# Kernel tuning notes

Hardware: AMD Instinct MI355X
Metric: run time of the kernel (lower is better)

## Reference

```python
import jax, jax.numpy as jnp
import numpy as np

B, N, D = 8, 1024, 256   # batch, nodes, input_size
H, HO = 4, 64            # nhead, hidden_size/nhead
T = 5                    # number of edge types (len(edges))
NEG = -1e9
EPS = 1e-6


def setup_inputs() -> dict:
    key = jax.random.key(0)
    ks = jax.random.split(key, 6)
    nodes_embed = jax.random.normal(ks[0], (B, N, D), dtype=jnp.float32)
    node_adj = jax.random.randint(ks[1], (B, N, N), 0, T + 1)  # values 0..T, 0 = no edge
    # per-head projection W: xavier-ish scale
    W = jax.random.normal(ks[2], (H, D, HO), dtype=jnp.float32) * (1.0 / np.sqrt(D))
    # per-edge-type scoring linear (2*HO -> 1), split into src/dst halves
    a_src = jax.random.normal(ks[3], (H, T, HO), dtype=jnp.float32) * 0.1
    a_dst = jax.random.normal(ks[4], (H, T, HO), dtype=jnp.float32) * 0.1
    bias = jnp.zeros((H, HO), dtype=jnp.float32)
    ln_gamma = jnp.ones((H, HO), dtype=jnp.float32)
    ln_beta = jnp.zeros((H, HO), dtype=jnp.float32)
    return {
        'nodes_embed': nodes_embed,
        'node_adj': node_adj,
        'W': W,
        'a_src': a_src,
        'a_dst': a_dst,
        'bias': bias,
        'ln_gamma': ln_gamma,
        'ln_beta': ln_beta,
    }


def reference(nodes_embed, node_adj, W, a_src, a_dst, bias, ln_gamma, ln_beta):
    # h: [B, H, N, HO] -- all heads projected at once
    h = jnp.einsum('bnd,hde->bhne', nodes_embed, W)
    # The torch code concatenates [h_i, h_j] and applies a (2*HO -> 1) linear per
    # edge type; that equals e_src[t, i] + e_dst[t, j] with the linear weight split
    # into src/dst halves. Avoids materializing the O(N^2 * 2*HO) concat tensor.
    e_src = jnp.einsum('bhne,hte->bhtn', h, a_src)  # [B, H, T, N]
    e_dst = jnp.einsum('bhne,hte->bhtn', h, a_dst)  # [B, H, T, N]
    n_types = a_src.shape[1]
    weight = jnp.zeros(h.shape[:2] + (h.shape[2], h.shape[2]), dtype=h.dtype)  # [B,H,N,N]
    for t in range(n_types):  # small fixed loop over edge types
        mask = (node_adj == t + 1).astype(h.dtype)[:, None]  # [B,1,N,N]
        weight = weight + mask * (e_src[:, :, t, :, None] + e_dst[:, :, t, None, :])
    weight = jax.nn.leaky_relu(weight, negative_slope=0.01)
    weight = jnp.where(node_adj[:, None] == 0, NEG, weight)
    attention = jax.nn.softmax(weight, axis=-1)  # [B,H,N,N]
    dst = jnp.einsum('bhij,bhje->bhie', attention, h) + bias[None, :, None, :]
    out = jax.nn.relu(dst) + h  # dropout is identity (p=0)
    # per-head LayerNorm over HO, eps=1e-6 (biased variance, as torch)
    mu = out.mean(axis=-1, keepdims=True)
    var = out.var(axis=-1, keepdims=True)
    out = (out - mu) / jnp.sqrt(var + EPS) * ln_gamma[None, :, None, :] + ln_beta[None, :, None, :]
    # concat heads: [B,H,N,HO] -> [B,N,H*HO]
    b, hh, n, e = out.shape
    return out.transpose(0, 2, 1, 3).reshape(b, n, hh * e)
```

## Files before the change

kernel.cpp:

```cpp
#include <hip/hip_runtime.h>
#include <hip/hip_bf16.h>

#define Bn 8
#define Nn 1024
#define Dn 256
#define Hn 4
#define HOn 64
#define Tn 5
#define WTR 80
#define EDS 134

typedef short bf16x8 __attribute__((ext_vector_type(8)));
typedef float f32x4 __attribute__((ext_vector_type(4)));

__device__ __forceinline__ float b2f(unsigned short u) {
    unsigned x = ((unsigned)u) << 16;
    float f;
    __builtin_memcpy(&f, &x, 4);
    return f;
}
__device__ __forceinline__ unsigned bfr(float f) {
    unsigned u;
    __builtin_memcpy(&u, &f, 4);
    return (u + 0x7FFFu + ((u >> 16) & 1u)) >> 16;
}
__device__ __forceinline__ unsigned short f2b(float f) { return (unsigned short)bfr(f); }

__device__ __forceinline__ float fast_exp2(float x) {
#if __has_builtin(__builtin_amdgcn_exp2f)
    return __builtin_amdgcn_exp2f(x);
#else
    float r;
    asm("v_exp_f32 %0, %1" : "=v"(r) : "v"(x));
    return r;
#endif
}

__global__ __launch_bounds__(256) void k_signal(float* __restrict__ out, int n) {
    int i = blockIdx.x * 256 + threadIdx.x;
    if (i < n) out[i] = 100.0f;
}

__global__ __launch_bounds__(256) void k_transpose_w(const float* __restrict__ W,
                                                     const float* __restrict__ a_src,
                                                     const float* __restrict__ a_dst,
                                                     unsigned short* __restrict__ WT) {
    __shared__ float tile[64][65];
    int h = blockIdx.x >> 2;
    int d0 = (blockIdx.x & 3) * 64;
    int c0 = threadIdx.x & 63;
    int r0 = threadIdx.x >> 6;
#pragma unroll
    for (int r = 0; r < 16; r++) {
        int d = r * 4 + r0;
        tile[d][c0] = W[((size_t)(h * Dn + d0 + d)) * HOn + c0];
    }
    __syncthreads();
#pragma unroll
    for (int r = 0; r < 16; r++) {
        int e = r * 4 + r0;
        WT[((size_t)(h * WTR + e)) * Dn + d0 + c0] = f2b(tile[c0][e]);
    }
    for (int t = r0; t < 2 * Tn; t += 4) {
        const float* av = (t < Tn) ? (a_src + (h * Tn + t) * HOn)
                                   : (a_dst + (h * Tn + t - Tn) * HOn);
        float s = 0.f;
#pragma unroll
        for (int e = 0; e < HOn; e++) s += tile[c0][e] * av[e];
        WT[((size_t)(h * WTR + 64 + t)) * Dn + d0 + c0] = f2b(s);
    }
    for (int rr = 74 + r0; rr < WTR; rr += 4)
        WT[((size_t)(h * WTR + rr)) * Dn + d0 + c0] = 0;
}

__global__ __launch_bounds__(256) void k_proj(const float* __restrict__ X,
                                              const unsigned short* __restrict__ WT,
                                              const int* __restrict__ adj,
                                              unsigned short* __restrict__ hT,
                                              float* __restrict__ e_src,
                                              float* __restrict__ e_dst,
                                              unsigned* __restrict__ adjp) {
    int tid = threadIdx.x;
    int w = tid >> 6;
    int lane = tid & 63;
    int quad = lane >> 4;
    int l15 = lane & 15;
    int b = blockIdx.x >> 6;
    int i0 = (blockIdx.x & 63) * 16;
    int h = w;
    int bh = b * Hn + h;

    {
        const int* arow = adj + ((size_t)(b * Nn + i0)) * Nn;
        unsigned* aout = adjp + ((size_t)(b * Nn + i0)) * Nn / 4;
#pragma unroll 4
        for (int k = 0; k < 16; k++) {
            int idx = tid + k * 256;
            int4 v = *(const int4*)(arow + (size_t)idx * 4);
            unsigned pk = (unsigned)(v.x & 0xFF) | ((unsigned)(v.y & 0xFF) << 8) |
                          ((unsigned)(v.z & 0xFF) << 16) | ((unsigned)(v.w & 0xFF) << 24);
            aout[idx] = pk;
        }
    }

    bf16x8 Bx[8];
    const float* xf = X + ((size_t)(b * Nn + i0 + l15)) * Dn + quad * 8;
#pragma unroll
    for (int kc = 0; kc < 8; kc++) {
        union { bf16x8 v; unsigned u[4]; } uu;
        const float4* xp = (const float4*)(xf + kc * 32);
        float4 A0 = xp[0], A1 = xp[1];
        __hip_bfloat162 h0 = __float22bfloat162_rn(make_float2(A0.x, A0.y));
        __hip_bfloat162 h1 = __float22bfloat162_rn(make_float2(A0.z, A0.w));
        __hip_bfloat162 h2 = __float22bfloat162_rn(make_float2(A1.x, A1.y));
        __hip_bfloat162 h3 = __float22bfloat162_rn(make_float2(A1.z, A1.w));
        __builtin_memcpy(&uu.u[0], &h0, 4);
        __builtin_memcpy(&uu.u[1], &h1, 4);
        __builtin_memcpy(&uu.u[2], &h2, 4);
        __builtin_memcpy(&uu.u[3], &h3, 4);
        Bx[kc] = uu.v;
    }

    f32x4 acc[5] = {{0.f, 0.f, 0.f, 0.f}, {0.f, 0.f, 0.f, 0.f}, {0.f, 0.f, 0.f, 0.f},
                    {0.f, 0.f, 0.f, 0.f}, {0.f, 0.f, 0.f, 0.f}};
    const unsigned short* wbase = WT + (size_t)h * WTR * Dn;
#pragma unroll
    for (int kc = 0; kc < 8; kc++) {
#pragma unroll
        for (int et = 0; et < 5; et++) {
            bf16x8 Aw = *(const bf16x8*)(wbase + (size_t)(et * 16 + l15) * Dn + kc * 32 + quad * 8);
            acc[et] = __builtin_amdgcn_mfma_f32_16x16x32_bf16(Aw, Bx[kc], acc[et], 0, 0, 0);
        }
    }

#pragma unroll
    for (int et = 0; et < 4; et++) {
#pragma unroll
        for (int reg = 0; reg < 4; reg++) {
            int e = et * 16 + quad * 4 + reg;
            hT[((size_t)bh * HOn + e) * Nn + i0 + l15] = f2b(acc[et][reg]);
        }
    }
#pragma unroll
    for (int reg = 0; reg < 4; reg++) {
        int t = quad * 4 + reg;
        if (t < Tn)
            e_src[((size_t)bh * Tn + t) * Nn + i0 + l15] = acc[4][reg] * 1.4426950408889634f;
        else if (t < 2 * Tn)
            e_dst[((size_t)bh * Tn + (t - Tn)) * Nn + i0 + l15] = acc[4][reg] * 1.4426950408889634f;
    }
}

__global__ __launch_bounds__(512) void k_attn(const unsigned char* __restrict__ adjp,
                                              const float* __restrict__ e_src,
                                              const float* __restrict__ e_dst,
                                              const unsigned short* __restrict__ hT,
                                              const float* __restrict__ bias,
                                              const float* __restrict__ gamma,
                                              const float* __restrict__ beta,
                                              float* __restrict__ out) {
    __shared__ __align__(16) unsigned short p_lds[8][16][136];
    __shared__ float es2[4][16][8];
    __shared__ float l_lds[8][16];
    __shared__ __align__(16) float ed_lds[8][6 * EDS];
    float* macc = (float*)&p_lds[4][0][0];

    int tid = threadIdx.x;
    int w = tid >> 6;
    int lane = tid & 63;
    int quad = lane >> 4;
    int l15 = lane & 15;
    int hh = w & 3;
    int half = w >> 2;
    int b = blockIdx.x >> 6;
    int i0 = (blockIdx.x & 63) * 16;
    int bh = b * Hn + hh;
    int J0 = half * 512;

    const unsigned char* adj_base = adjp + ((size_t)(b * Nn + i0)) * Nn + J0;
    const float* edst = e_dst + (size_t)bh * Tn * Nn + J0;
    const unsigned short* hTb = hT + (size_t)bh * HOn * Nn;

    int c0 = 2 * lane;
    int c0w = c0 + (c0 >> 5);
    float* edw = &ed_lds[w][0];

    f32x4 acc[4] = {{0.f, 0.f, 0.f, 0.f}, {0.f, 0.f, 0.f, 0.f},
                    {0.f, 0.f, 0.f, 0.f}, {0.f, 0.f, 0.f, 0.f}};
    f32x4 accl = {0.f, 0.f, 0.f, 0.f};
    bf16x8 ONES;
    {
        short o = (short)0x3F80;
        ONES = (bf16x8){o, o, o, o, o, o, o, o};
    }

    edw[c0w] = -3e38f;
    edw[c0w + 1] = -3e38f;

    unsigned bufA[4], bufB[4];
#pragma unroll
    for (int r = 0; r < 4; r++)
        bufA[r] = *(const unsigned short*)(adj_base + (size_t)r * Nn + c0);
    float2 edr[Tn];
#pragma unroll
    for (int t = 0; t < Tn; t++) edr[t] = *(const float2*)(edst + t * Nn + c0);

    if (w < 4) {
        const float* esrc = e_src + (size_t)bh * Tn * Nn;
#pragma unroll
        for (int idx = lane; idx < 96; idx += 64) {
            int t = idx >> 4, row = idx & 15;
            es2[w][row][t] = t ? esrc[(t - 1) * Nn + i0 + row] : 0.f;
        }
    }
    __syncthreads();

#define P1ROW(ROW, AV)                                                          \
    {                                                                           \
        int a0 = (int)((AV) & 0xFFu);                                           \
        int a1 = (int)((AV) >> 8);                                              \
        float e0 = es2[hh][ROW][a0];                                            \
        float e1 = es2[hh][ROW][a1];                                            \
        float d0 = edw[a0 * EDS + c0w];                                         \
        float d1 = edw[a1 * EDS + c0w + 1];                                     \
        float x0 = e0 + d0; x0 = fmaxf(x0, 0.01f * x0);                         \
        float x1 = e1 + d1; x1 = fmaxf(x1, 0.01f * x1);                         \
        float p0 = fast_exp2(x0);                                               \
        float p1 = fast_exp2(x1);                                               \
        __hip_bfloat162 pp = __float22bfloat162_rn(make_float2(p0, p1));        \
        unsigned pu; __builtin_memcpy(&pu, &pp, 4);                             \
        *(unsigned*)(&p_lds[w][ROW][2 * lane]) = pu;                            \
    }

#pragma unroll 1
    for (int c = 0; c < 4; c++) {
        int jc = c * 128;
#pragma unroll
        for (int t = 0; t < Tn; t++) {
            int wi = (t + 1) * EDS + c0w;
            edw[wi] = edr[t].x;
            edw[wi + 1] = edr[t].y;
        }
#pragma unroll
        for (int r = 0; r < 4; r++)
            bufB[r] = *(const unsigned short*)(adj_base + (size_t)(4 + r) * Nn + jc + c0);
#pragma unroll
        for (int r = 0; r < 4; r++) P1ROW(r, bufA[r]);
#pragma unroll
        for (int r = 0; r < 4; r++)
            bufA[r] = *(const unsigned short*)(adj_base + (size_t)(8 + r) * Nn + jc + c0);
        if (c < 3) {
#pragma unroll
            for (int t = 0; t < Tn; t++)
                edr[t] = *(const float2*)(edst + t * Nn + jc + 128 + c0);
        }
#pragma unroll
        for (int r = 0; r < 4; r++) P1ROW(4 + r, bufB[r]);
#pragma unroll
        for (int r = 0; r < 4; r++)
            bufB[r] = *(const unsigned short*)(adj_base + (size_t)(12 + r) * Nn + jc + c0);
#pragma unroll
        for (int r = 0; r < 4; r++) P1ROW(8 + r, bufA[r]);
        if (c < 3) {
#pragma unroll
            for (int r = 0; r < 4; r++)
                bufA[r] = *(const unsigned short*)(adj_base + (size_t)r * Nn + jc + 128 + c0);
        }
#pragma unroll
        for (int r = 0; r < 4; r++) P1ROW(12 + r, bufB[r]);
#pragma unroll
        for (int k = 0; k < 4; k++) {
            bf16x8 Afr = *(const bf16x8*)(&p_lds[w][l15][k * 32 + quad * 8]);
            accl = __builtin_amdgcn_mfma_f32_16x16x32_bf16(Afr, ONES, accl, 0, 0, 0);
#pragma unroll
            for (int et = 0; et < 4; et++) {
                bf16x8 Bf = *(const bf16x8*)(hTb + (size_t)(et * 16 + l15) * Nn + J0 + jc + k * 32 + quad * 8);
                acc[et] = __builtin_amdgcn_mfma_f32_16x16x32_bf16(Afr, Bf, acc[et], 0, 0, 0);
            }
        }
    }
#undef P1ROW

    if (l15 == 0) {
#pragma unroll
        for (int reg = 0; reg < 4; reg++) l_lds[w][quad * 4 + reg] = accl[reg];
    }
    __syncthreads();
    if (w >= 4) {
#pragma unroll
        for (int et = 0; et < 4; et++)
#pragma unroll
            for (int reg = 0; reg < 4; reg++)
                macc[((hh * 16) + quad * 4 + reg) * 64 + et * 16 + l15] = acc[et][reg];
    }
    __syncthreads();
    if (w >= 4) return;

    float bv[4], gv[4], bev[4];
#pragma unroll
    for (int et = 0; et < 4; et++) {
        int e = et * 16 + l15;
        bv[et] = bias[hh * HOn + e];
        gv[et] = gamma[hh * HOn + e];
        bev[et] = beta[hh * HOn + e];
    }
#pragma unroll
    for (int reg = 0; reg < 4; reg++) {
        int r = quad * 4 + reg;
        int i = i0 + r;
        float lw = l_lds[w][r] + l_lds[w + 4][r];
        float linv = 1.f / fmaxf(lw, 1e-30f);
        float dv[4];
        float s = 0.f, ss = 0.f;
#pragma unroll
        for (int et = 0; et < 4; et++) {
            int e = et * 16 + l15;
            float v = (acc[et][reg] + macc[((hh * 16) + r) * 64 + e]) * linv + bv[et];
            v = (v > 0.f) ? v : 0.f;
            v += b2f(hTb[(size_t)e * Nn + i]);
            dv[et] = v;
            s += v;
            ss += v * v;
        }
#pragma unroll
        for (int off = 8; off; off >>= 1) {
            s += __shfl_xor(s, off);
            ss += __shfl_xor(ss, off);
        }
        float mean = s * (1.f / 64.f);
        float var = ss * (1.f / 64.f) - mean * mean;
        float rstd = rsqrtf(var + 1e-6f);
#pragma unroll
        for (int et = 0; et < 4; et++) {
            int e = et * 16 + l15;
            float o = (dv[et] - mean) * rstd * gv[et] + bev[et];
            out[((size_t)(b * Nn + i)) * (Hn * HOn) + hh * HOn + e] = o;
        }
    }
}

extern "C" void kernel_launch(void* const* d_in, const int* in_sizes, int n_in,
                              void* d_out, int out_size, void* d_ws, size_t ws_size,
                              hipStream_t stream) {
    const float* X = (const float*)d_in[0];
    const int* adj = (const int*)d_in[1];
    const float* W = (const float*)d_in[2];
    const float* a_src = (const float*)d_in[3];
    const float* a_dst = (const float*)d_in[4];
    const float* bias = (const float*)d_in[5];
    const float* gamma = (const float*)d_in[6];
    const float* beta = (const float*)d_in[7];
    float* out = (float*)d_out;

    char* ws = (char*)d_ws;
    size_t off = 0;
    unsigned short* hT = (unsigned short*)(ws + off);  off += (size_t)Bn * Hn * Nn * HOn * 2;
    unsigned short* WT = (unsigned short*)(ws + off);  off += (size_t)Hn * WTR * Dn * 2;
    float* e_src = (float*)(ws + off);                 off += (size_t)Bn * Hn * Tn * Nn * 4;
    float* e_dst = (float*)(ws + off);                 off += (size_t)Bn * Hn * Tn * Nn * 4;
    unsigned char* adjp = (unsigned char*)(ws + off);  off += (size_t)Bn * Nn * Nn;

    if (ws_size < off) {
        k_signal<<<(out_size + 255) / 256, 256, 0, stream>>>(out, out_size);
        return;
    }

    k_transpose_w<<<Hn * (Dn / 64), 256, 0, stream>>>(W, a_src, a_dst, WT);
    k_proj<<<Bn * (Nn / 16), 256, 0, stream>>>(X, WT, adj, hT, e_src, e_dst, (unsigned*)adjp);
    k_attn<<<Bn * (Nn / 16), 512, 0, stream>>>(adjp, e_src, e_dst, hT, bias, gamma, beta, out);
}
```

Measured before the change: 151.4 us.

## Prefetch full 16-row adjacency chunk one iteration ahead and drop LDS padding

Replaces the staggered 4-row double-buffer of adjacency loads with a full 16-row prefetch of the next column chunk, issued before the current chunk is processed. This gives the global loads a whole iteration of latency hiding instead of a quarter-chunk. It also removes the bank-conflict padding from the e_dst LDS tile (stride 134 to 128, no per-32 skew), simplifying addressing but possibly reintroducing LDS bank conflicts on the gathered reads. The larger prefetch buffers raise register pressure.

```diff
diff --git a/kernel.cpp b/kernel.cpp
--- a/kernel.cpp
+++ b/kernel.cpp
@@ -8,7 +8,7 @@
 #define HOn 64
 #define Tn 5
 #define WTR 80
-#define EDS 134
+#define EDS 128
 
 typedef short bf16x8 __attribute__((ext_vector_type(8)));
 typedef float f32x4 __attribute__((ext_vector_type(4)));
@@ -182,7 +182,6 @@
     const unsigned short* hTb = hT + (size_t)bh * HOn * Nn;
 
     int c0 = 2 * lane;
-    int c0w = c0 + (c0 >> 5);
     float* edw = &ed_lds[w][0];
 
     f32x4 acc[4] = {{0.f, 0.f, 0.f, 0.f}, {0.f, 0.f, 0.f, 0.f},
@@ -194,13 +193,13 @@
         ONES = (bf16x8){o, o, o, o, o, o, o, o};
     }
 
-    edw[c0w] = -3e38f;
-    edw[c0w + 1] = -3e38f;
-
-    unsigned bufA[4], bufB[4];
-#pragma unroll
-    for (int r = 0; r < 4; r++)
-        bufA[r] = *(const unsigned short*)(adj_base + (size_t)r * Nn + c0);
+    edw[c0] = -3e38f;
+    edw[c0 + 1] = -3e38f;
+
+    unsigned adjC[16], adjN[16];
+#pragma unroll
+    for (int r = 0; r < 16; r++)
+        adjC[r] = *(const unsigned short*)(adj_base + (size_t)r * Nn + c0);
     float2 edr[Tn];
 #pragma unroll
     for (int t = 0; t < Tn; t++) edr[t] = *(const float2*)(edst + t * Nn + c0);
@@ -221,8 +220,8 @@
         int a1 = (int)((AV) >> 8);                                              \
         float e0 = es2[hh][ROW][a0];                                            \
         float e1 = es2[hh][ROW][a1];                                            \
-        float d0 = edw[a0 * EDS + c0w];                                         \
-        float d1 = edw[a1 * EDS + c0w + 1];                                     \
+        float d0 = edw[a0 * EDS + c0];                                          \
+        float d1 = edw[a1 * EDS + c0 + 1];                                      \
         float x0 = e0 + d0; x0 = fmaxf(x0, 0.01f * x0);                         \
         float x1 = e1 + d1; x1 = fmaxf(x1, 0.01f * x1);                         \
         float p0 = fast_exp2(x0);                                               \
@@ -237,37 +236,20 @@
         int jc = c * 128;
 #pragma unroll
         for (int t = 0; t < Tn; t++) {
-            int wi = (t + 1) * EDS + c0w;
+            int wi = (t + 1) * EDS + c0;
             edw[wi] = edr[t].x;
             edw[wi + 1] = edr[t].y;
         }
-#pragma unroll
-        for (int r = 0; r < 4; r++)
-            bufB[r] = *(const unsigned short*)(adj_base + (size_t)(4 + r) * Nn + jc + c0);
-#pragma unroll
-        for (int r = 0; r < 4; r++) P1ROW(r, bufA[r]);
-#pragma unroll
-        for (int r = 0; r < 4; r++)
-            bufA[r] = *(const unsigned short*)(adj_base + (size_t)(8 + r) * Nn + jc + c0);
         if (c < 3) {
+#pragma unroll
+            for (int r = 0; r < 16; r++)
+                adjN[r] = *(const unsigned short*)(adj_base + (size_t)r * Nn + jc + 128 + c0);
 #pragma unroll
             for (int t = 0; t < Tn; t++)
                 edr[t] = *(const float2*)(edst + t * Nn + jc + 128 + c0);
         }
 #pragma unroll
-        for (int r = 0; r < 4; r++) P1ROW(4 + r, bufB[r]);
-#pragma unroll
-        for (int r = 0; r < 4; r++)
-            bufB[r] = *(const unsigned short*)(adj_base + (size_t)(12 + r) * Nn + jc + c0);
-#pragma unroll
-        for (int r = 0; r < 4; r++) P1ROW(8 + r, bufA[r]);
-        if (c < 3) {
-#pragma unroll
-            for (int r = 0; r < 4; r++)
-                bufA[r] = *(const unsigned short*)(adj_base + (size_t)r * Nn + jc + 128 + c0);
-        }
-#pragma unroll
-        for (int r = 0; r < 4; r++) P1ROW(12 + r, bufB[r]);
+        for (int r = 0; r < 16; r++) P1ROW(r, adjC[r]);
 #pragma unroll
         for (int k = 0; k < 4; k++) {
             bf16x8 Afr = *(const bf16x8*)(&p_lds[w][l15][k * 32 + quad * 8]);
@@ -277,6 +259,10 @@
                 bf16x8 Bf = *(const bf16x8*)(hTb + (size_t)(et * 16 + l15) * Nn + J0 + jc + k * 32 + quad * 8);
                 acc[et] = __builtin_amdgcn_mfma_f32_16x16x32_bf16(Afr, Bf, acc[et], 0, 0, 0);
             }
+        }
+        if (c < 3) {
+#pragma unroll
+            for (int r = 0; r < 16; r++) adjC[r] = adjN[r];
         }
     }
 #undef P1ROW
```

Result: no change. 149.8 us (-1.0%).
